# Kernel tuning notes

Measured on AMD Instinct MI355X. Metric: run time of the kernel, lower is better.

## Reference

```python
import jax, jax.numpy as jnp
import numpy as np

B, NQ, NK, QS, KS, H, VD = 16, 64, 512, 256, 256, 256, 256


def setup_inputs() -> dict:
    key = jax.random.key(0)
    k1, k2, k3, k4, k5, k6, k7 = jax.random.split(key, 7)
    return {
        "queries": jax.random.normal(k1, (B, NQ, QS), dtype=jnp.float32),
        "keys": jax.random.normal(k2, (B, NK, KS), dtype=jnp.float32),
        "values": jax.random.normal(k3, (B, NK, VD), dtype=jnp.float32),
        "valid_lens": jax.random.randint(k4, (B,), 1, NK + 1, dtype=jnp.int32),
        # learned params (nn.Linear with bias=False): W_q [QS,H], W_k [KS,H], w_v [H]
        "W_q": jax.random.normal(k5, (QS, H), dtype=jnp.float32) / np.sqrt(QS),
        "W_k": jax.random.normal(k6, (KS, H), dtype=jnp.float32) / np.sqrt(KS),
        "w_v": jax.random.normal(k7, (H,), dtype=jnp.float32) / np.sqrt(H),
    }


def reference(queries, keys, values, valid_lens, W_q, W_k, w_v):
    # project: q [B,nq,H], k [B,nk,H]
    q = jnp.einsum("bqd,dh->bqh", queries, W_q)
    k = jnp.einsum("bkd,dh->bkh", keys, W_k)
    # broadcast-add -> tanh -> score reduction via w_v: [B,nq,nk]
    features = jnp.tanh(q[:, :, None, :] + k[:, None, :, :])  # [B,nq,nk,H]
    scores = jnp.einsum("bqkh,h->bqk", features, w_v)
    # masked softmax over keys (positions >= valid_len masked out)
    mask = jnp.arange(scores.shape[-1])[None, None, :] < valid_lens[:, None, None]
    scores = jnp.where(mask, scores, -1e6)
    attn = jax.nn.softmax(scores, axis=-1)
    # weighted sum of values (dropout p=0 / eval mode => identity)
    return jnp.einsum("bqk,bkv->bqv", attn, values)
```

## Files before the change

kernel.cpp:

```cpp
#include <hip/hip_runtime.h>
#include <hip/hip_bf16.h>

#define BB 16
#define NQ 64
#define NK 512
#define HD 256

typedef __attribute__((ext_vector_type(8))) short short8;
typedef __attribute__((ext_vector_type(4))) float f32x4;

__device__ __forceinline__ ushort bf16_rne(float v) {
    unsigned u = __float_as_uint(v);
    return (ushort)((u + 0x7FFFu + ((u >> 16) & 1u)) >> 16);
}
__device__ __forceinline__ float bf16_to_f(ushort h) {
    return __uint_as_float(((unsigned)h) << 16);
}

__global__ __launch_bounds__(256) void convert_split(
    const float* __restrict__ q, const float* __restrict__ k,
    const float* __restrict__ wq, const float* __restrict__ wk,
    ushort* __restrict__ qh, ushort* __restrict__ ql,
    ushort* __restrict__ kh, ushort* __restrict__ kl,
    ushort* __restrict__ wqh, ushort* __restrict__ wql,
    ushort* __restrict__ wkh, ushort* __restrict__ wkl)
{
    const int idx = blockIdx.x * 256 + threadIdx.x;
    if (blockIdx.x < 2304) {
        int e = idx * 4;
        const float* src; ushort *dh, *dl; int off;
        if (e < 1024 * 256) { src = q; dh = qh; dl = ql; off = e; }
        else { src = k; dh = kh; dl = kl; off = e - 1024 * 256; }
        float4 v = *(const float4*)&src[off];
        float fv[4] = {v.x, v.y, v.z, v.w};
        ushort hh[4], ll[4];
        #pragma unroll
        for (int c = 0; c < 4; ++c) {
            hh[c] = bf16_rne(fv[c]);
            ll[c] = bf16_rne(fv[c] - bf16_to_f(hh[c]));
        }
        *(ushort4*)&dh[off] = make_ushort4(hh[0], hh[1], hh[2], hh[3]);
        *(ushort4*)&dl[off] = make_ushort4(ll[0], ll[1], ll[2], ll[3]);
    } else {
        int widx = idx - 2304 * 256;
        const float* W; ushort *wh, *wl;
        if (widx < 16384) { W = wq; wh = wqh; wl = wql; }
        else { W = wk; wh = wkh; wl = wkl; widx -= 16384; }
        int n  = widx >> 6;
        int k4 = (widx & 63) * 4;
        ushort hh[4], ll[4];
        #pragma unroll
        for (int c = 0; c < 4; ++c) {
            float v = W[(k4 + c) * 256 + n];
            hh[c] = bf16_rne(v);
            ll[c] = bf16_rne(v - bf16_to_f(hh[c]));
        }
        *(ushort4*)&wh[n * 256 + k4] = make_ushort4(hh[0], hh[1], hh[2], hh[3]);
        *(ushort4*)&wl[n * 256 + k4] = make_ushort4(ll[0], ll[1], ll[2], ll[3]);
    }
}

__global__ __launch_bounds__(256, 2) void proj_mfma2(
    const ushort* __restrict__ qh, const ushort* __restrict__ ql,
    const ushort* __restrict__ kh, const ushort* __restrict__ kl,
    const ushort* __restrict__ wqh, const ushort* __restrict__ wql,
    const ushort* __restrict__ wkh, const ushort* __restrict__ wkl,
    float* __restrict__ qp, float* __restrict__ kp, float scale)
{
    __shared__ ushort AsH[128 * 64], AsL[128 * 64];
    __shared__ ushort BsH[64 * 64],  BsL[64 * 64];

    const ushort *Ah, *Al, *Bh, *Bl; float* C; int rows0;
    if (blockIdx.x < 8) { Ah = qh; Al = ql; Bh = wqh; Bl = wql; C = qp; rows0 = blockIdx.x * 128; }
    else                { Ah = kh; Al = kl; Bh = wkh; Bl = wkl; C = kp; rows0 = (blockIdx.x - 8) * 128; }
    const int cols0 = blockIdx.y * 64;

    const int t = threadIdx.x, lane = t & 63, wave = t >> 6;
    const int quad = lane >> 4, l15 = lane & 15;
    const int lr = lane >> 3;
    const int cg = (lane & 7) ^ lr;
    const int swz0 = quad ^ (l15 & 7);
    const int swz1 = (quad + 4) ^ (l15 & 7);

    f32x4 acc[2][4];
    #pragma unroll
    for (int i = 0; i < 2; ++i)
        #pragma unroll
        for (int j = 0; j < 4; ++j)
            acc[i][j] = (f32x4){0.f, 0.f, 0.f, 0.f};

    short8 rAh[4], rAl[4], rBh[2], rBl[2];
    #pragma unroll
    for (int i = 0; i < 4; ++i) {
        size_t g = (size_t)(rows0 + (wave * 4 + i) * 8 + lr) * 256 + cg * 8;
        rAh[i] = *(const short8*)&Ah[g];
        rAl[i] = *(const short8*)&Al[g];
    }
    #pragma unroll
    for (int j = 0; j < 2; ++j) {
        size_t g = (size_t)(cols0 + (wave * 2 + j) * 8 + lr) * 256 + cg * 8;
        rBh[j] = *(const short8*)&Bh[g];
        rBl[j] = *(const short8*)&Bl[g];
    }

    for (int k0 = 0; k0 < 256; k0 += 64) {
        __syncthreads();
        #pragma unroll
        for (int i = 0; i < 4; ++i) {
            int ci = (wave * 4 + i) * 64 + lane;
            *(short8*)&AsH[ci * 8] = rAh[i];
            *(short8*)&AsL[ci * 8] = rAl[i];
        }
        #pragma unroll
        for (int j = 0; j < 2; ++j) {
            int ci = (wave * 2 + j) * 64 + lane;
            *(short8*)&BsH[ci * 8] = rBh[j];
            *(short8*)&BsL[ci * 8] = rBl[j];
        }
        __syncthreads();

        if (k0 + 64 < 256) {
            #pragma unroll
            for (int i = 0; i < 4; ++i) {
                size_t g = (size_t)(rows0 + (wave * 4 + i) * 8 + lr) * 256 + k0 + 64 + cg * 8;
                rAh[i] = *(const short8*)&Ah[g];
                rAl[i] = *(const short8*)&Al[g];
            }
            #pragma unroll
            for (int j = 0; j < 2; ++j) {
                size_t g = (size_t)(cols0 + (wave * 2 + j) * 8 + lr) * 256 + k0 + 64 + cg * 8;
                rBh[j] = *(const short8*)&Bh[g];
                rBl[j] = *(const short8*)&Bl[g];
            }
        }

        #pragma unroll
        for (int ks = 0; ks < 2; ++ks) {
            const int s = ks ? swz1 : swz0;
            short8 aH[2], aL[2], bH[4], bL[4];
            #pragma unroll
            for (int ms = 0; ms < 2; ++ms) {
                int r = wave * 32 + ms * 16 + l15;
                aH[ms] = *(const short8*)&AsH[r * 64 + s * 8];
                aL[ms] = *(const short8*)&AsL[r * 64 + s * 8];
            }
            #pragma unroll
            for (int ns = 0; ns < 4; ++ns) {
                int n = ns * 16 + l15;
                bH[ns] = *(const short8*)&BsH[n * 64 + s * 8];
                bL[ns] = *(const short8*)&BsL[n * 64 + s * 8];
            }
            #pragma unroll
            for (int ms = 0; ms < 2; ++ms)
                #pragma unroll
                for (int ns = 0; ns < 4; ++ns)
                    acc[ms][ns] = __builtin_amdgcn_mfma_f32_16x16x32_bf16(aH[ms], bH[ns], acc[ms][ns], 0, 0, 0);
            #pragma unroll
            for (int ms = 0; ms < 2; ++ms)
                #pragma unroll
                for (int ns = 0; ns < 4; ++ns)
                    acc[ms][ns] = __builtin_amdgcn_mfma_f32_16x16x32_bf16(aL[ms], bH[ns], acc[ms][ns], 0, 0, 0);
            #pragma unroll
            for (int ms = 0; ms < 2; ++ms)
                #pragma unroll
                for (int ns = 0; ns < 4; ++ns)
                    acc[ms][ns] = __builtin_amdgcn_mfma_f32_16x16x32_bf16(aH[ms], bL[ns], acc[ms][ns], 0, 0, 0);
        }
    }

    #pragma unroll
    for (int ms = 0; ms < 2; ++ms) {
        int rbase = rows0 + wave * 32 + ms * 16 + quad * 4;
        #pragma unroll
        for (int ns = 0; ns < 4; ++ns) {
            int col = cols0 + ns * 16 + l15;
            #pragma unroll
            for (int r = 0; r < 4; ++r)
                C[(size_t)(rbase + r) * 256 + col] = acc[ms][ns][r] * scale;
        }
    }
}

__global__ __launch_bounds__(256) void score_pv_seg(
    const float* __restrict__ qp,
    const float* __restrict__ kp,
    const float* __restrict__ values,
    const int*   __restrict__ vlens,
    const float* __restrict__ w_v,
    float* __restrict__ pO,
    float* __restrict__ pM,
    float* __restrict__ pL)
{
    __shared__ float Ps[2][64];
    __shared__ float part[4][2][HD];

    const int b     = blockIdx.x & 15;
    const int qpair = blockIdx.x >> 4;
    const int seg   = blockIdx.y;
    const int vl    = vlens[b];
    if (seg * 64 >= vl) return;

    const int t = threadIdx.x, lane = t & 63, wave = t >> 6;
    const int keyLoc = lane >> 4, ch = lane & 15;

    const float* q0 = qp + ((size_t)b * NQ + qpair * 2) * HD;
    float eqa[16], eqb[16];
    float4 wf[4];
    float Wsum = 0.f;
    #pragma unroll
    for (int m = 0; m < 4; ++m) {
        float4 a  = *(const float4*)&q0[ch * 4 + m * 64];
        float4 bq = *(const float4*)&q0[HD + ch * 4 + m * 64];
        wf[m] = *(const float4*)&w_v[ch * 4 + m * 64];
        eqa[m * 4 + 0] = __builtin_amdgcn_exp2f(a.x);
        eqa[m * 4 + 1] = __builtin_amdgcn_exp2f(a.y);
        eqa[m * 4 + 2] = __builtin_amdgcn_exp2f(a.z);
        eqa[m * 4 + 3] = __builtin_amdgcn_exp2f(a.w);
        eqb[m * 4 + 0] = __builtin_amdgcn_exp2f(bq.x);
        eqb[m * 4 + 1] = __builtin_amdgcn_exp2f(bq.y);
        eqb[m * 4 + 2] = __builtin_amdgcn_exp2f(bq.z);
        eqb[m * 4 + 3] = __builtin_amdgcn_exp2f(bq.w);
        Wsum += (wf[m].x + wf[m].y) + (wf[m].z + wf[m].w);
    }
    Wsum += __shfl_xor(Wsum, 1);
    Wsum += __shfl_xor(Wsum, 2);
    Wsum += __shfl_xor(Wsum, 4);
    Wsum += __shfl_xor(Wsum, 8);

    const float* kbase = kp + ((size_t)b * NK + seg * 64) * HD;
    #pragma unroll
    for (int it = 0; it < 4; ++it) {
        const int nloc = it * 16 + wave * 4 + keyLoc;
        const float* krow = kbase + (size_t)nloc * HD + ch * 4;
        float4 kk[4];
        #pragma unroll
        for (int m = 0; m < 4; ++m) kk[m] = *(const float4*)&krow[m * 64];

        float s0 = 0.f, s1 = 0.f;
        #pragma unroll
        for (int m = 0; m < 4; ++m) {
            float kv[4]  = {kk[m].x, kk[m].y, kk[m].z, kk[m].w};
            float wv4[4] = {wf[m].x, wf[m].y, wf[m].z, wf[m].w};
            #pragma unroll
            for (int c = 0; c < 4; ++c) {
                float ek = __builtin_amdgcn_exp2f(kv[c]);
                float r0 = __builtin_amdgcn_rcpf(fmaf(eqa[m * 4 + c], ek, 1.f));
                float r1 = __builtin_amdgcn_rcpf(fmaf(eqb[m * 4 + c], ek, 1.f));
                s0 = fmaf(wv4[c], r0, s0);
                s1 = fmaf(wv4[c], r1, s1);
            }
        }
        s0 += __shfl_xor(s0, 1); s0 += __shfl_xor(s0, 2);
        s0 += __shfl_xor(s0, 4); s0 += __shfl_xor(s0, 8);
        s1 += __shfl_xor(s1, 1); s1 += __shfl_xor(s1, 2);
        s1 += __shfl_xor(s1, 4); s1 += __shfl_xor(s1, 8);
        if (ch == 0) {
            const bool masked = (seg * 64 + nloc >= vl);
            Ps[0][nloc] = masked ? -1e6f : fmaf(-2.f, s0, Wsum);
            Ps[1][nloc] = masked ? -1e6f : fmaf(-2.f, s1, Wsum);
        }
    }
    __syncthreads();

    const float L2E = 1.4426950408889634f;
    if (wave < 2) {
        float s = Ps[wave][lane];
        float m = s;
        #pragma unroll
        for (int off = 32; off; off >>= 1) m = fmaxf(m, __shfl_xor(m, off));
        float e = __builtin_amdgcn_exp2f((s - m) * L2E);
        float l = e;
        #pragma unroll
        for (int off = 32; off; off >>= 1) l += __shfl_xor(l, off);
        Ps[wave][lane] = e;
        if (lane == 0) {
            size_t mi = ((size_t)(b * 32 + qpair) * 8 + seg) * 2 + wave;
            pM[mi] = m;
            pL[mi] = l;
        }
    }
    __syncthreads();

    f32x4 acc0 = (f32x4){0.f, 0.f, 0.f, 0.f};
    f32x4 acc1 = (f32x4){0.f, 0.f, 0.f, 0.f};
    const float* vbase = values + ((size_t)b * NK + seg * 64) * HD;
    #pragma unroll
    for (int i = 0; i < 16; ++i) {
        const int k = wave * 16 + i;
        float p0 = Ps[0][k];
        float p1 = Ps[1][k];
        float4 v = *(const float4*)&vbase[(size_t)k * HD + lane * 4];
        acc0[0] = fmaf(p0, v.x, acc0[0]); acc0[1] = fmaf(p0, v.y, acc0[1]);
        acc0[2] = fmaf(p0, v.z, acc0[2]); acc0[3] = fmaf(p0, v.w, acc0[3]);
        acc1[0] = fmaf(p1, v.x, acc1[0]); acc1[1] = fmaf(p1, v.y, acc1[1]);
        acc1[2] = fmaf(p1, v.z, acc1[2]); acc1[3] = fmaf(p1, v.w, acc1[3]);
    }
    *(f32x4*)&part[wave][0][lane * 4] = acc0;
    *(f32x4*)&part[wave][1][lane * 4] = acc1;
    __syncthreads();

    if (wave < 2) {
        float4 p0 = *(const float4*)&part[0][wave][lane * 4];
        float4 p1 = *(const float4*)&part[1][wave][lane * 4];
        float4 p2 = *(const float4*)&part[2][wave][lane * 4];
        float4 p3 = *(const float4*)&part[3][wave][lane * 4];
        f32x4 o;
        o[0] = (p0.x + p1.x) + (p2.x + p3.x);
        o[1] = (p0.y + p1.y) + (p2.y + p3.y);
        o[2] = (p0.z + p1.z) + (p2.z + p3.z);
        o[3] = (p0.w + p1.w) + (p2.w + p3.w);
        size_t ob = (((size_t)(b * 32 + qpair) * 8 + seg) * 2 + wave) * 256;
        *(f32x4*)&pO[ob + lane * 4] = o;
    }
}

__global__ __launch_bounds__(256) void combine_seg(
    const float* __restrict__ pO, const float* __restrict__ pM,
    const float* __restrict__ pL, const int* __restrict__ vlens,
    float* __restrict__ out)
{
    const int b  = blockIdx.x >> 6;
    const int q  = blockIdx.x & 63;
    const int t  = threadIdx.x;
    const int vl = vlens[b];
    const int nc = (vl + 63) >> 6;
    const int qpair = q >> 1, q2 = q & 1;
    const float L2E = 1.4426950408889634f;

    const size_t base = (size_t)(b * 32 + qpair) * 8;

    float mi[8], li[8];
    float m = -3e38f;
    #pragma unroll
    for (int i = 0; i < 8; ++i) {
        if (i < nc) {
            mi[i] = pM[(base + i) * 2 + q2];
            li[i] = pL[(base + i) * 2 + q2];
            m = fmaxf(m, mi[i]);
        }
    }
    float L = 0.f, wi[8];
    #pragma unroll
    for (int i = 0; i < 8; ++i) {
        if (i < nc) {
            wi[i] = __builtin_amdgcn_exp2f((mi[i] - m) * L2E);
            L = fmaf(li[i], wi[i], L);
        }
    }
    float acc = 0.f;
    #pragma unroll
    for (int i = 0; i < 8; ++i) {
        if (i < nc) acc = fmaf(wi[i], pO[((base + i) * 2 + q2) * 256 + t], acc);
    }
    out[((size_t)(b * 64 + q)) * 256 + t] = acc * __builtin_amdgcn_rcpf(L);
}

extern "C" void kernel_launch(void* const* d_in, const int* in_sizes, int n_in,
                              void* d_out, int out_size, void* d_ws, size_t ws_size,
                              hipStream_t stream) {
    const float* queries = (const float*)d_in[0];
    const float* keys    = (const float*)d_in[1];
    const float* values  = (const float*)d_in[2];
    const int*   vlens   = (const int*)d_in[3];
    const float* W_q     = (const float*)d_in[4];
    const float* W_k     = (const float*)d_in[5];
    const float* w_v     = (const float*)d_in[6];
    float* out = (float*)d_out;

    float*  kp  = (float*)d_ws;
    float*  qp  = kp + (size_t)BB * NK * HD;
    float*  pO  = qp + (size_t)BB * NQ * HD;
    float*  pM  = pO + (size_t)BB * 32 * 8 * 2 * 256;
    float*  pL  = pM + (size_t)BB * 32 * 8 * 2;
    ushort* qh  = (ushort*)(pL + (size_t)BB * 32 * 8 * 2);
    ushort* ql  = qh  + 1024 * 256;
    ushort* kh  = ql  + 1024 * 256;
    ushort* kl  = kh  + 8192 * 256;
    ushort* wqh = kl  + 8192 * 256;
    ushort* wql = wqh + 65536;
    ushort* wkh = wql + 65536;
    ushort* wkl = wkh + 65536;

    const float SC = 2.885390081777927f;

    convert_split<<<dim3(2432), 256, 0, stream>>>(queries, keys, W_q, W_k,
                                                  qh, ql, kh, kl,
                                                  wqh, wql, wkh, wkl);
    proj_mfma2<<<dim3(72, 4), 256, 0, stream>>>(qh, ql, kh, kl,
                                                wqh, wql, wkh, wkl,
                                                qp, kp, SC);
    score_pv_seg<<<dim3(512, 8), 256, 0, stream>>>(qp, kp, values, vlens, w_v,
                                                   pO, pM, pL);
    combine_seg<<<dim3(BB * NQ), 256, 0, stream>>>(pO, pM, pL, vlens, out);
}
```

Before: 120.2 us.

## Fuse activation bf16 split into projection GEMM and tile eight queries per score block

```diff
diff --git a/kernel.cpp b/kernel.cpp
--- a/kernel.cpp
+++ b/kernel.cpp
@@ -17,171 +17,133 @@
     return __uint_as_float(((unsigned)h) << 16);
 }
 
-__global__ __launch_bounds__(256) void convert_split(
-    const float* __restrict__ q, const float* __restrict__ k,
+__global__ __launch_bounds__(256) void wconv(
     const float* __restrict__ wq, const float* __restrict__ wk,
-    ushort* __restrict__ qh, ushort* __restrict__ ql,
-    ushort* __restrict__ kh, ushort* __restrict__ kl,
     ushort* __restrict__ wqh, ushort* __restrict__ wql,
     ushort* __restrict__ wkh, ushort* __restrict__ wkl)
 {
-    const int idx = blockIdx.x * 256 + threadIdx.x;
-    if (blockIdx.x < 2304) {
-        int e = idx * 4;
-        const float* src; ushort *dh, *dl; int off;
-        if (e < 1024 * 256) { src = q; dh = qh; dl = ql; off = e; }
-        else { src = k; dh = kh; dl = kl; off = e - 1024 * 256; }
-        float4 v = *(const float4*)&src[off];
-        float fv[4] = {v.x, v.y, v.z, v.w};
-        ushort hh[4], ll[4];
-        #pragma unroll
-        for (int c = 0; c < 4; ++c) {
-            hh[c] = bf16_rne(fv[c]);
-            ll[c] = bf16_rne(fv[c] - bf16_to_f(hh[c]));
-        }
-        *(ushort4*)&dh[off] = make_ushort4(hh[0], hh[1], hh[2], hh[3]);
-        *(ushort4*)&dl[off] = make_ushort4(ll[0], ll[1], ll[2], ll[3]);
-    } else {
-        int widx = idx - 2304 * 256;
-        const float* W; ushort *wh, *wl;
-        if (widx < 16384) { W = wq; wh = wqh; wl = wql; }
-        else { W = wk; wh = wkh; wl = wkl; widx -= 16384; }
-        int n  = widx >> 6;
-        int k4 = (widx & 63) * 4;
-        ushort hh[4], ll[4];
-        #pragma unroll
-        for (int c = 0; c < 4; ++c) {
-            float v = W[(k4 + c) * 256 + n];
-            hh[c] = bf16_rne(v);
-            ll[c] = bf16_rne(v - bf16_to_f(hh[c]));
-        }
-        *(ushort4*)&wh[n * 256 + k4] = make_ushort4(hh[0], hh[1], hh[2], hh[3]);
-        *(ushort4*)&wl[n * 256 + k4] = make_ushort4(ll[0], ll[1], ll[2], ll[3]);
-    }
-}
-
-__global__ __launch_bounds__(256, 2) void proj_mfma2(
-    const ushort* __restrict__ qh, const ushort* __restrict__ ql,
-    const ushort* __restrict__ kh, const ushort* __restrict__ kl,
+    int widx = blockIdx.x * 256 + threadIdx.x;
+    const float* W; ushort *wh, *wl;
+    if (widx < 16384) { W = wq; wh = wqh; wl = wql; }
+    else { W = wk; wh = wkh; wl = wkl; widx -= 16384; }
+    int n  = widx >> 6;
+    int k4 = (widx & 63) * 4;
+    ushort hh[4], ll[4];
+    #pragma unroll
+    for (int c = 0; c < 4; ++c) {
+        float v = W[(k4 + c) * 256 + n];
+        hh[c] = bf16_rne(v);
+        ll[c] = bf16_rne(v - bf16_to_f(hh[c]));
+    }
+    *(ushort4*)&wh[n * 256 + k4] = make_ushort4(hh[0], hh[1], hh[2], hh[3]);
+    *(ushort4*)&wl[n * 256 + k4] = make_ushort4(ll[0], ll[1], ll[2], ll[3]);
+}
+
+__global__ __launch_bounds__(256, 2) void proj_fused(
+    const float* __restrict__ queries, const float* __restrict__ keys,
     const ushort* __restrict__ wqh, const ushort* __restrict__ wql,
     const ushort* __restrict__ wkh, const ushort* __restrict__ wkl,
     float* __restrict__ qp, float* __restrict__ kp, float scale)
 {
-    __shared__ ushort AsH[128 * 64], AsL[128 * 64];
-    __shared__ ushort BsH[64 * 64],  BsL[64 * 64];
-
-    const ushort *Ah, *Al, *Bh, *Bl; float* C; int rows0;
-    if (blockIdx.x < 8) { Ah = qh; Al = ql; Bh = wqh; Bl = wql; C = qp; rows0 = blockIdx.x * 128; }
-    else                { Ah = kh; Al = kl; Bh = wkh; Bl = wkl; C = kp; rows0 = (blockIdx.x - 8) * 128; }
+    __shared__ ushort AsH[64 * 64], AsL[64 * 64];
+    __shared__ ushort BsH[64 * 64], BsL[64 * 64];
+
+    const float* A; const ushort *Bh, *Bl; float* C; int rows0;
+    const int bx = blockIdx.x;
+    if (bx < 16) { A = queries; Bh = wqh; Bl = wql; C = qp; rows0 = bx * 64; }
+    else         { A = keys;    Bh = wkh; Bl = wkl; C = kp; rows0 = (bx - 16) * 64; }
     const int cols0 = blockIdx.y * 64;
 
     const int t = threadIdx.x, lane = t & 63, wave = t >> 6;
     const int quad = lane >> 4, l15 = lane & 15;
-    const int lr = lane >> 3;
-    const int cg = (lane & 7) ^ lr;
-    const int swz0 = quad ^ (l15 & 7);
-    const int swz1 = (quad + 4) ^ (l15 & 7);
-
-    f32x4 acc[2][4];
-    #pragma unroll
-    for (int i = 0; i < 2; ++i)
-        #pragma unroll
-        for (int j = 0; j < 4; ++j)
-            acc[i][j] = (f32x4){0.f, 0.f, 0.f, 0.f};
-
-    short8 rAh[4], rAl[4], rBh[2], rBl[2];
-    #pragma unroll
-    for (int i = 0; i < 4; ++i) {
-        size_t g = (size_t)(rows0 + (wave * 4 + i) * 8 + lr) * 256 + cg * 8;
-        rAh[i] = *(const short8*)&Ah[g];
-        rAl[i] = *(const short8*)&Al[g];
-    }
-    #pragma unroll
-    for (int j = 0; j < 2; ++j) {
-        size_t g = (size_t)(cols0 + (wave * 2 + j) * 8 + lr) * 256 + cg * 8;
-        rBh[j] = *(const short8*)&Bh[g];
-        rBl[j] = *(const short8*)&Bl[g];
-    }
+    const int sr  = t >> 2;
+    const int sc2 = (t & 3) * 2;
+
+    f32x4 acc[4];
+    #pragma unroll
+    for (int j = 0; j < 4; ++j) acc[j] = (f32x4){0.f, 0.f, 0.f, 0.f};
 
     for (int k0 = 0; k0 < 256; k0 += 64) {
+        const float* arow = &A[(size_t)(rows0 + sr) * 256 + k0 + sc2 * 8];
+        float4 a0 = *(const float4*)&arow[0];
+        float4 a1 = *(const float4*)&arow[4];
+        float4 a2 = *(const float4*)&arow[8];
+        float4 a3 = *(const float4*)&arow[12];
+        const ushort* bhp = &Bh[(size_t)(cols0 + sr) * 256 + k0 + sc2 * 8];
+        const ushort* blp = &Bl[(size_t)(cols0 + sr) * 256 + k0 + sc2 * 8];
+        short8 b0h = *(const short8*)&bhp[0];
+        short8 b1h = *(const short8*)&bhp[8];
+        short8 b0l = *(const short8*)&blp[0];
+        short8 b1l = *(const short8*)&blp[8];
+
         __syncthreads();
-        #pragma unroll
-        for (int i = 0; i < 4; ++i) {
-            int ci = (wave * 4 + i) * 64 + lane;
-            *(short8*)&AsH[ci * 8] = rAh[i];
-            *(short8*)&AsL[ci * 8] = rAl[i];
-        }
-        #pragma unroll
-        for (int j = 0; j < 2; ++j) {
-            int ci = (wave * 2 + j) * 64 + lane;
-            *(short8*)&BsH[ci * 8] = rBh[j];
-            *(short8*)&BsL[ci * 8] = rBl[j];
+
+        float av[16] = {a0.x, a0.y, a0.z, a0.w, a1.x, a1.y, a1.z, a1.w,
+                        a2.x, a2.y, a2.z, a2.w, a3.x, a3.y, a3.z, a3.w};
+        short8 ah0, ah1, al0, al1;
+        #pragma unroll
+        for (int e = 0; e < 8; ++e) {
+            ushort h0 = bf16_rne(av[e]);
+            ushort h1 = bf16_rne(av[8 + e]);
+            ah0[e] = (short)h0;
+            ah1[e] = (short)h1;
+            al0[e] = (short)bf16_rne(av[e] - bf16_to_f(h0));
+            al1[e] = (short)bf16_rne(av[8 + e] - bf16_to_f(h1));
+        }
+        {
+            int s0 = sr * 8 + ((sc2 + 0) ^ (sr & 7));
+            int s1 = sr * 8 + ((sc2 + 1) ^ (sr & 7));
+            *(short8*)&AsH[s0 * 8] = ah0;
+            *(short8*)&AsH[s1 * 8] = ah1;
+            *(short8*)&AsL[s0 * 8] = al0;
+            *(short8*)&AsL[s1 * 8] = al1;
+            *(short8*)&BsH[s0 * 8] = b0h;
+            *(short8*)&BsH[s1 * 8] = b1h;
+            *(short8*)&BsL[s0 * 8] = b0l;
+            *(short8*)&BsL[s1 * 8] = b1l;
         }
         __syncthreads();
 
-        if (k0 + 64 < 256) {
-            #pragma unroll
-            for (int i = 0; i < 4; ++i) {
-                size_t g = (size_t)(rows0 + (wave * 4 + i) * 8 + lr) * 256 + k0 + 64 + cg * 8;
-                rAh[i] = *(const short8*)&Ah[g];
-                rAl[i] = *(const short8*)&Al[g];
-            }
-            #pragma unroll
-            for (int j = 0; j < 2; ++j) {
-                size_t g = (size_t)(cols0 + (wave * 2 + j) * 8 + lr) * 256 + k0 + 64 + cg * 8;
-                rBh[j] = *(const short8*)&Bh[g];
-                rBl[j] = *(const short8*)&Bl[g];
-            }
-        }
-
         #pragma unroll
         for (int ks = 0; ks < 2; ++ks) {
-            const int s = ks ? swz1 : swz0;
-            short8 aH[2], aL[2], bH[4], bL[4];
-            #pragma unroll
-            for (int ms = 0; ms < 2; ++ms) {
-                int r = wave * 32 + ms * 16 + l15;
-                aH[ms] = *(const short8*)&AsH[r * 64 + s * 8];
-                aL[ms] = *(const short8*)&AsL[r * 64 + s * 8];
+            const int c = ks * 4 + quad;
+            short8 aH, aL, bH[4], bL[4];
+            {
+                int r = wave * 16 + l15;
+                int slot = r * 8 + (c ^ (r & 7));
+                aH = *(const short8*)&AsH[slot * 8];
+                aL = *(const short8*)&AsL[slot * 8];
             }
             #pragma unroll
             for (int ns = 0; ns < 4; ++ns) {
                 int n = ns * 16 + l15;
-                bH[ns] = *(const short8*)&BsH[n * 64 + s * 8];
-                bL[ns] = *(const short8*)&BsL[n * 64 + s * 8];
+                int slot = n * 8 + (c ^ (n & 7));
+                bH[ns] = *(const short8*)&BsH[slot * 8];
+                bL[ns] = *(const short8*)&BsL[slot * 8];
             }
             #pragma unroll
-            for (int ms = 0; ms < 2; ++ms)
-                #pragma unroll
-                for (int ns = 0; ns < 4; ++ns)
-                    acc[ms][ns] = __builtin_amdgcn_mfma_f32_16x16x32_bf16(aH[ms], bH[ns], acc[ms][ns], 0, 0, 0);
+            for (int ns = 0; ns < 4; ++ns)
+                acc[ns] = __builtin_amdgcn_mfma_f32_16x16x32_bf16(aH, bH[ns], acc[ns], 0, 0, 0);
             #pragma unroll
-            for (int ms = 0; ms < 2; ++ms)
-                #pragma unroll
-                for (int ns = 0; ns < 4; ++ns)
-                    acc[ms][ns] = __builtin_amdgcn_mfma_f32_16x16x32_bf16(aL[ms], bH[ns], acc[ms][ns], 0, 0, 0);
+            for (int ns = 0; ns < 4; ++ns)
+                acc[ns] = __builtin_amdgcn_mfma_f32_16x16x32_bf16(aL, bH[ns], acc[ns], 0, 0, 0);
             #pragma unroll
-            for (int ms = 0; ms < 2; ++ms)
-                #pragma unroll
-                for (int ns = 0; ns < 4; ++ns)
-                    acc[ms][ns] = __builtin_amdgcn_mfma_f32_16x16x32_bf16(aH[ms], bL[ns], acc[ms][ns], 0, 0, 0);
-        }
-    }
-
-    #pragma unroll
-    for (int ms = 0; ms < 2; ++ms) {
-        int rbase = rows0 + wave * 32 + ms * 16 + quad * 4;
-        #pragma unroll
-        for (int ns = 0; ns < 4; ++ns) {
-            int col = cols0 + ns * 16 + l15;
-            #pragma unroll
-            for (int r = 0; r < 4; ++r)
-                C[(size_t)(rbase + r) * 256 + col] = acc[ms][ns][r] * scale;
-        }
-    }
-}
-
-__global__ __launch_bounds__(256) void score_pv_seg(
+            for (int ns = 0; ns < 4; ++ns)
+                acc[ns] = __builtin_amdgcn_mfma_f32_16x16x32_bf16(aH, bL[ns], acc[ns], 0, 0, 0);
+        }
+    }
+
+    const int rbase = rows0 + wave * 16 + quad * 4;
+    #pragma unroll
+    for (int ns = 0; ns < 4; ++ns) {
+        int col = cols0 + ns * 16 + l15;
+        #pragma unroll
+        for (int r = 0; r < 4; ++r)
+            C[(size_t)(rbase + r) * 256 + col] = acc[ns][r] * scale;
+    }
+}
+
+__global__ __launch_bounds__(256) void score_pv_seg2(
     const float* __restrict__ qp,
     const float* __restrict__ kp,
     const float* __restrict__ values,
@@ -191,130 +153,139 @@
     float* __restrict__ pM,
     float* __restrict__ pL)
 {
-    __shared__ float Ps[2][64];
-    __shared__ float part[4][2][HD];
-
-    const int b     = blockIdx.x & 15;
-    const int qpair = blockIdx.x >> 4;
-    const int seg   = blockIdx.y;
-    const int vl    = vlens[b];
+    __shared__ float eq[8][260];
+    __shared__ float wv[HD];
+    __shared__ float Ps[8][66];
+    __shared__ float part[4][8][260];
+
+    const int b   = blockIdx.x & 15;
+    const int qt  = blockIdx.x >> 4;
+    const int seg = blockIdx.y;
+    const int vl  = vlens[b];
     if (seg * 64 >= vl) return;
 
     const int t = threadIdx.x, lane = t & 63, wave = t >> 6;
-    const int keyLoc = lane >> 4, ch = lane & 15;
-
-    const float* q0 = qp + ((size_t)b * NQ + qpair * 2) * HD;
-    float eqa[16], eqb[16];
-    float4 wf[4];
-    float Wsum = 0.f;
-    #pragma unroll
-    for (int m = 0; m < 4; ++m) {
-        float4 a  = *(const float4*)&q0[ch * 4 + m * 64];
-        float4 bq = *(const float4*)&q0[HD + ch * 4 + m * 64];
-        wf[m] = *(const float4*)&w_v[ch * 4 + m * 64];
-        eqa[m * 4 + 0] = __builtin_amdgcn_exp2f(a.x);
-        eqa[m * 4 + 1] = __builtin_amdgcn_exp2f(a.y);
-        eqa[m * 4 + 2] = __builtin_amdgcn_exp2f(a.z);
-        eqa[m * 4 + 3] = __builtin_amdgcn_exp2f(a.w);
-        eqb[m * 4 + 0] = __builtin_amdgcn_exp2f(bq.x);
-        eqb[m * 4 + 1] = __builtin_amdgcn_exp2f(bq.y);
-        eqb[m * 4 + 2] = __builtin_amdgcn_exp2f(bq.z);
-        eqb[m * 4 + 3] = __builtin_amdgcn_exp2f(bq.w);
-        Wsum += (wf[m].x + wf[m].y) + (wf[m].z + wf[m].w);
-    }
-    Wsum += __shfl_xor(Wsum, 1);
-    Wsum += __shfl_xor(Wsum, 2);
-    Wsum += __shfl_xor(Wsum, 4);
-    Wsum += __shfl_xor(Wsum, 8);
-
-    const float* kbase = kp + ((size_t)b * NK + seg * 64) * HD;
-    #pragma unroll
-    for (int it = 0; it < 4; ++it) {
-        const int nloc = it * 16 + wave * 4 + keyLoc;
-        const float* krow = kbase + (size_t)nloc * HD + ch * 4;
-        float4 kk[4];
-        #pragma unroll
-        for (int m = 0; m < 4; ++m) kk[m] = *(const float4*)&krow[m * 64];
-
-        float s0 = 0.f, s1 = 0.f;
-        #pragma unroll
-        for (int m = 0; m < 4; ++m) {
-            float kv[4]  = {kk[m].x, kk[m].y, kk[m].z, kk[m].w};
-            float wv4[4] = {wf[m].x, wf[m].y, wf[m].z, wf[m].w};
-            #pragma unroll
-            for (int c = 0; c < 4; ++c) {
-                float ek = __builtin_amdgcn_exp2f(kv[c]);
-                float r0 = __builtin_amdgcn_rcpf(fmaf(eqa[m * 4 + c], ek, 1.f));
-                float r1 = __builtin_amdgcn_rcpf(fmaf(eqb[m * 4 + c], ek, 1.f));
-                s0 = fmaf(wv4[c], r0, s0);
-                s1 = fmaf(wv4[c], r1, s1);
-            }
-        }
-        s0 += __shfl_xor(s0, 1); s0 += __shfl_xor(s0, 2);
-        s0 += __shfl_xor(s0, 4); s0 += __shfl_xor(s0, 8);
-        s1 += __shfl_xor(s1, 1); s1 += __shfl_xor(s1, 2);
-        s1 += __shfl_xor(s1, 4); s1 += __shfl_xor(s1, 8);
-        if (ch == 0) {
-            const bool masked = (seg * 64 + nloc >= vl);
-            Ps[0][nloc] = masked ? -1e6f : fmaf(-2.f, s0, Wsum);
-            Ps[1][nloc] = masked ? -1e6f : fmaf(-2.f, s1, Wsum);
-        }
-    }
+
+    const float* qsrc = qp + ((size_t)b * NQ + qt * 8) * HD;
+    #pragma unroll
+    for (int i = 0; i < 2; ++i) {
+        int idx = i * 256 + t;
+        int row = idx >> 6, c4 = (idx & 63) * 4;
+        float4 v = *(const float4*)&qsrc[(size_t)row * HD + c4];
+        eq[row][c4 + 0] = __builtin_amdgcn_exp2f(v.x);
+        eq[row][c4 + 1] = __builtin_amdgcn_exp2f(v.y);
+        eq[row][c4 + 2] = __builtin_amdgcn_exp2f(v.z);
+        eq[row][c4 + 3] = __builtin_amdgcn_exp2f(v.w);
+    }
+    if (t < 64) *(float4*)&wv[t * 4] = *(const float4*)&w_v[t * 4];
     __syncthreads();
 
+    float Wsum;
+    {
+        float ws = wv[lane] + wv[lane + 64] + wv[lane + 128] + wv[lane + 192];
+        #pragma unroll
+        for (int off = 32; off; off >>= 1) ws += __shfl_xor(ws, off);
+        Wsum = ws;
+    }
+
+    const int key = wave * 16 + (lane >> 2);
+    const int ch  = lane & 3;
+    const int kg  = seg * 64 + key;
+    const float* krow = kp + ((size_t)b * NK + kg) * HD + ch * 4;
+
+    float s[8] = {0.f, 0.f, 0.f, 0.f, 0.f, 0.f, 0.f, 0.f};
+    #pragma unroll
+    for (int j = 0; j < 16; ++j) {
+        const int h = j * 16 + ch * 4;
+        float4 k4 = *(const float4*)&krow[j * 16];
+        float4 w4 = *(const float4*)&wv[h];
+        float ek0 = __builtin_amdgcn_exp2f(k4.x);
+        float ek1 = __builtin_amdgcn_exp2f(k4.y);
+        float ek2 = __builtin_amdgcn_exp2f(k4.z);
+        float ek3 = __builtin_amdgcn_exp2f(k4.w);
+        #pragma unroll
+        for (int qi = 0; qi < 8; ++qi) {
+            float4 q4 = *(const float4*)&eq[qi][h];
+            float t0 = fmaf(w4.x, __builtin_amdgcn_rcpf(fmaf(q4.x, ek0, 1.f)), s[qi]);
+            t0 = fmaf(w4.y, __builtin_amdgcn_rcpf(fmaf(q4.y, ek1, 1.f)), t0);
+            t0 = fmaf(w4.z, __builtin_amdgcn_rcpf(fmaf(q4.z, ek2, 1.f)), t0);
+            s[qi] = fmaf(w4.w, __builtin_amdgcn_rcpf(fmaf(q4.w, ek3, 1.f)), t0);
+        }
+    }
+    #pragma unroll
+    for (int qi = 0; qi < 8; ++qi) {
+        s[qi] += __shfl_xor(s[qi], 1);
+        s[qi] += __shfl_xor(s[qi], 2);
+    }
+    if (ch == 0) {
+        const bool masked = (kg >= vl);
+        #pragma unroll
+        for (int qi = 0; qi < 8; ++qi)
+            Ps[qi][key] = masked ? -1e6f : fmaf(-2.f, s[qi], Wsum);
+    }
+    __syncthreads();
+
     const float L2E = 1.4426950408889634f;
-    if (wave < 2) {
-        float s = Ps[wave][lane];
-        float m = s;
+    #pragma unroll
+    for (int r = 0; r < 2; ++r) {
+        const int row = wave * 2 + r;
+        float sv = Ps[row][lane];
+        float m = sv;
         #pragma unroll
         for (int off = 32; off; off >>= 1) m = fmaxf(m, __shfl_xor(m, off));
-        float e = __builtin_amdgcn_exp2f((s - m) * L2E);
+        float e = __builtin_amdgcn_exp2f((sv - m) * L2E);
         float l = e;
         #pragma unroll
         for (int off = 32; off; off >>= 1) l += __shfl_xor(l, off);
-        Ps[wave][lane] = e;
+        Ps[row][lane] = e;
         if (lane == 0) {
-            size_t mi = ((size_t)(b * 32 + qpair) * 8 + seg) * 2 + wave;
+            size_t mi = (((size_t)(b * 8 + qt) * 8 + seg)) * 8 + row;
             pM[mi] = m;
             pL[mi] = l;
         }
     }
     __syncthreads();
 
-    f32x4 acc0 = (f32x4){0.f, 0.f, 0.f, 0.f};
-    f32x4 acc1 = (f32x4){0.f, 0.f, 0.f, 0.f};
-    const float* vbase = values + ((size_t)b * NK + seg * 64) * HD;
+    f32x4 acc[8];
+    #pragma unroll
+    for (int qi = 0; qi < 8; ++qi) acc[qi] = (f32x4){0.f, 0.f, 0.f, 0.f};
+    const float* vbase = values + ((size_t)b * NK + seg * 64 + wave * 16) * HD;
     #pragma unroll
     for (int i = 0; i < 16; ++i) {
-        const int k = wave * 16 + i;
-        float p0 = Ps[0][k];
-        float p1 = Ps[1][k];
-        float4 v = *(const float4*)&vbase[(size_t)k * HD + lane * 4];
-        acc0[0] = fmaf(p0, v.x, acc0[0]); acc0[1] = fmaf(p0, v.y, acc0[1]);
-        acc0[2] = fmaf(p0, v.z, acc0[2]); acc0[3] = fmaf(p0, v.w, acc0[3]);
-        acc1[0] = fmaf(p1, v.x, acc1[0]); acc1[1] = fmaf(p1, v.y, acc1[1]);
-        acc1[2] = fmaf(p1, v.z, acc1[2]); acc1[3] = fmaf(p1, v.w, acc1[3]);
-    }
-    *(f32x4*)&part[wave][0][lane * 4] = acc0;
-    *(f32x4*)&part[wave][1][lane * 4] = acc1;
+        float4 v = *(const float4*)&vbase[(size_t)i * HD + lane * 4];
+        #pragma unroll
+        for (int qi = 0; qi < 8; ++qi) {
+            float p = Ps[qi][wave * 16 + i];
+            acc[qi][0] = fmaf(p, v.x, acc[qi][0]);
+            acc[qi][1] = fmaf(p, v.y, acc[qi][1]);
+            acc[qi][2] = fmaf(p, v.z, acc[qi][2]);
+            acc[qi][3] = fmaf(p, v.w, acc[qi][3]);
+        }
+    }
+    #pragma unroll
+    for (int qi = 0; qi < 8; ++qi)
+        *(f32x4*)&part[wave][qi][lane * 4] = acc[qi];
     __syncthreads();
 
-    if (wave < 2) {
-        float4 p0 = *(const float4*)&part[0][wave][lane * 4];
-        float4 p1 = *(const float4*)&part[1][wave][lane * 4];
-        float4 p2 = *(const float4*)&part[2][wave][lane * 4];
-        float4 p3 = *(const float4*)&part[3][wave][lane * 4];
-        f32x4 o;
-        o[0] = (p0.x + p1.x) + (p2.x + p3.x);
-        o[1] = (p0.y + p1.y) + (p2.y + p3.y);
-        o[2] = (p0.z + p1.z) + (p2.z + p3.z);
-        o[3] = (p0.w + p1.w) + (p2.w + p3.w);
-        size_t ob = (((size_t)(b * 32 + qpair) * 8 + seg) * 2 + wave) * 256;
-        *(f32x4*)&pO[ob + lane * 4] = o;
-    }
-}
-
-__global__ __launch_bounds__(256) void combine_seg(
+    const size_t ob = (((size_t)(b * 8 + qt) * 8 + seg)) * 8 * 256;
+    #pragma unroll
+    for (int i = 0; i < 2; ++i) {
+        int idx = i * 256 + t;
+        int qi = idx >> 6, c4 = (idx & 63) * 4;
+        float4 p0 = *(const float4*)&part[0][qi][c4];
+        float4 p1 = *(const float4*)&part[1][qi][c4];
+        float4 p2 = *(const float4*)&part[2][qi][c4];
+        float4 p3 = *(const float4*)&part[3][qi][c4];
+        float4 o;
+        o.x = (p0.x + p1.x) + (p2.x + p3.x);
+        o.y = (p0.y + p1.y) + (p2.y + p3.y);
+        o.z = (p0.z + p1.z) + (p2.z + p3.z);
+        o.w = (p0.w + p1.w) + (p2.w + p3.w);
+        *(float4*)&pO[ob + (size_t)qi * 256 + c4] = o;
+    }
+}
+
+__global__ __launch_bounds__(256) void combine_seg2(
     const float* __restrict__ pO, const float* __restrict__ pM,
     const float* __restrict__ pL, const int* __restrict__ vlens,
     float* __restrict__ out)
@@ -324,18 +295,18 @@
     const int t  = threadIdx.x;
     const int vl = vlens[b];
     const int nc = (vl + 63) >> 6;
-    const int qpair = q >> 1, q2 = q & 1;
+    const int qt = q >> 3, qi = q & 7;
     const float L2E = 1.4426950408889634f;
 
-    const size_t base = (size_t)(b * 32 + qpair) * 8;
+    const size_t base = (size_t)(b * 8 + qt) * 8;
 
     float mi[8], li[8];
     float m = -3e38f;
     #pragma unroll
     for (int i = 0; i < 8; ++i) {
         if (i < nc) {
-            mi[i] = pM[(base + i) * 2 + q2];
-            li[i] = pL[(base + i) * 2 + q2];
+            mi[i] = pM[(base + i) * 8 + qi];
+            li[i] = pL[(base + i) * 8 + qi];
             m = fmaxf(m, mi[i]);
         }
     }
@@ -350,7 +321,7 @@
     float acc = 0.f;
     #pragma unroll
     for (int i = 0; i < 8; ++i) {
-        if (i < nc) acc = fmaf(wi[i], pO[((base + i) * 2 + q2) * 256 + t], acc);
+        if (i < nc) acc = fmaf(wi[i], pO[((base + i) * 8 + qi) * 256 + t], acc);
     }
     out[((size_t)(b * 64 + q)) * 256 + t] = acc * __builtin_amdgcn_rcpf(L);
 }
@@ -370,26 +341,20 @@
     float*  kp  = (float*)d_ws;
     float*  qp  = kp + (size_t)BB * NK * HD;
     float*  pO  = qp + (size_t)BB * NQ * HD;
-    float*  pM  = pO + (size_t)BB * 32 * 8 * 2 * 256;
-    float*  pL  = pM + (size_t)BB * 32 * 8 * 2;
-    ushort* qh  = (ushort*)(pL + (size_t)BB * 32 * 8 * 2);
-    ushort* ql  = qh  + 1024 * 256;
-    ushort* kh  = ql  + 1024 * 256;
-    ushort* kl  = kh  + 8192 * 256;
-    ushort* wqh = kl  + 8192 * 256;
+    float*  pM  = pO + (size_t)BB * 8 * 8 * 8 * 256;
+    float*  pL  = pM + (size_t)BB * 8 * 8 * 8;
+    ushort* wqh = (ushort*)(pL + (size_t)BB * 8 * 8 * 8);
     ushort* wql = wqh + 65536;
     ushort* wkh = wql + 65536;
     ushort* wkl = wkh + 65536;
 
     const float SC = 2.885390081777927f;
 
-    convert_split<<<dim3(2432), 256, 0, stream>>>(queries, keys, W_q, W_k,
-                                                  qh, ql, kh, kl,
-                                                  wqh, wql, wkh, wkl);
-    proj_mfma2<<<dim3(72, 4), 256, 0, stream>>>(qh, ql, kh, kl,
-                                                wqh, wql, wkh, wkl,
-                                                qp, kp, SC);
-    score_pv_seg<<<dim3(512, 8), 256, 0, stream>>>(qp, kp, values, vlens, w_v,
-                                                   pO, pM, pL);
-    combine_seg<<<dim3(BB * NQ), 256, 0, stream>>>(pO, pM, pL, vlens, out);
-}
+    wconv<<<dim3(128), 256, 0, stream>>>(W_q, W_k, wqh, wql, wkh, wkl);
+    proj_fused<<<dim3(144, 4), 256, 0, stream>>>(queries, keys,
+                                                 wqh, wql, wkh, wkl,
+                                                 qp, kp, SC);
+    score_pv_seg2<<<dim3(128, 8), 256, 0, stream>>>(qp, kp, values, vlens, w_v,
+                                                    pO, pM, pL);
+    combine_seg2<<<dim3(BB * NQ), 256, 0, stream>>>(pO, pM, pL, vlens, out);
+}
```

Result: faster. 113.9 us (-5.2%).
